# Kernel optimization log

Measured on AMD Instinct MI355X. Metric: run time of the kernel, lower is better.

## Reference

```python
import jax, jax.numpy as jnp
import numpy as np
import math

B, DSET, DOUT, DH, H, L, M, C = 32, 512, 16, 1024, 16, 6, 127, 8
S = M + 1            # sos + maximum_components targets
DHEAD = DH // H
DIN = DSET + 1 + 2 * DOUT  # embedding input dim = 545
DTOK = 1 + 2 * DOUT        # per-step token dim = 33


def _pos_encoding(max_len, d):
    pos = np.arange(max_len, dtype=np.float32)[:, None]
    div = np.exp(np.arange(0, d, 2, dtype=np.float32) * (-math.log(10000.0) / d))
    pe = np.zeros((max_len, d), dtype=np.float32)
    pe[:, 0::2] = np.sin(pos * div)
    pe[:, 1::2] = np.cos(pos * div)
    return jnp.asarray(pe[None])  # [1, max_len, d]


def setup_inputs() -> dict:
    key = jax.random.key(0)
    ks = iter(jax.random.split(key, 64))
    def n(shape, s=0.02):
        return jax.random.normal(next(ks), shape, jnp.float32) * s
    return {
        "input": jax.random.normal(next(ks), (B, DSET), jnp.float32),
        "targets": jax.random.normal(next(ks), (B, M, DTOK), jnp.float32),
        "W_emb": n((DH, DIN)), "b_emb": jnp.zeros((DH,), jnp.float32),
        "sos": jax.random.normal(next(ks), (1, 1, DTOK), jnp.float32),
        "Wqkv": n((L, 3 * DH, DH)), "bqkv": jnp.zeros((L, 3 * DH), jnp.float32),
        "Wo": n((L, DH, DH)), "bo": jnp.zeros((L, DH), jnp.float32),
        "W1": n((L, DH, DH)), "b1": jnp.zeros((L, DH), jnp.float32),
        "W2": n((L, DH, DH)), "b2": jnp.zeros((L, DH), jnp.float32),
        "g1": jnp.ones((L, DH), jnp.float32), "be1": jnp.zeros((L, DH), jnp.float32),
        "g2": jnp.ones((L, DH), jnp.float32), "be2": jnp.zeros((L, DH), jnp.float32),
        "Wm": n((1, DH)), "bm": jnp.zeros((1,), jnp.float32),
        "Wpi_m": n((C, DH)), "bpi_m": jnp.zeros((C,), jnp.float32),
        "Wmu_m": n((C * DOUT, DH)), "bmu_m": jnp.zeros((C * DOUT,), jnp.float32),
        "Wsg_m": n((C * DOUT, DH)), "bsg_m": jnp.zeros((C * DOUT,), jnp.float32),
        "Wpi_v": n((C, DH)), "bpi_v": jnp.zeros((C,), jnp.float32),
        "Wmu_v": n((C * DOUT, DH)), "bmu_v": jnp.zeros((C * DOUT,), jnp.float32),
        "Wsg_v": n((C * DOUT, DH)), "bsg_v": jnp.zeros((C * DOUT,), jnp.float32),
    }


def _ln(x, g, b, eps=1e-5):
    m = x.mean(-1, keepdims=True)
    v = ((x - m) ** 2).mean(-1, keepdims=True)
    return (x - m) / jnp.sqrt(v + eps) * g + b


def _layer(x, Wqkv, bqkv, Wo, bo, W1, b1, W2, b2, g1, be1, g2, be2, causal):
    # PyTorch TransformerEncoderLayer (post-norm, relu, dropout=0)
    qkv = x @ Wqkv.T + bqkv                       # [B,S,3*DH]
    q, k, v = jnp.split(qkv, 3, axis=-1)
    q = q.reshape(B, -1, H, DHEAD)
    k = k.reshape(B, -1, H, DHEAD)
    v = v.reshape(B, -1, H, DHEAD)
    sc = jnp.einsum('bqhd,bkhd->bhqk', q, k) / math.sqrt(DHEAD)
    sc = jnp.where(causal, sc, -1e30)
    a = jax.nn.softmax(sc, -1)
    o = jnp.einsum('bhqk,bkhd->bqhd', a, v).reshape(B, -1, DH)
    x = _ln(x + o @ Wo.T + bo, g1, be1)
    ff = jax.nn.relu(x @ W1.T + b1) @ W2.T + b2
    return _ln(x + ff, g2, be2)


def _mdn(h, Wpi, bpi, Wmu, bmu, Wsg, bsg):
    pi = jax.nn.softmax(h @ Wpi.T + bpi, -1)                      # [B,M,C]
    mu = (h @ Wmu.T + bmu).reshape(h.shape[:-1] + (C, DOUT))      # [B,M,C,DOUT]
    var = jnp.exp(h @ Wsg.T + bsg).reshape(h.shape[:-1] + (C, DOUT))
    return pi, mu, var


def reference(input, targets, W_emb, b_emb, sos, Wqkv, bqkv, Wo, bo, W1, b1, W2, b2,
              g1, be1, g2, be2, Wm, bm, Wpi_m, bpi_m, Wmu_m, bmu_m, Wsg_m, bsg_m,
              Wpi_v, bpi_v, Wmu_v, bmu_v, Wsg_v, bsg_v):
    pe = _pos_encoding(3 * M, DH)
    tokens = jnp.broadcast_to(sos, (B, 1, DTOK))
    cond = jnp.broadcast_to(input[:, None, :], (B, S, DSET))
    seq = jnp.concatenate([tokens, targets], axis=1)              # [B,S,DTOK]
    x = jnp.concatenate([cond, seq], axis=-1) @ W_emb.T + b_emb
    x = x + pe[:, :S, :]
    causal = jnp.tril(jnp.ones((S, S), bool))[None, None]
    for i in range(L):
        x = _layer(x, Wqkv[i], bqkv[i], Wo[i], bo[i], W1[i], b1[i], W2[i], b2[i],
                   g1[i], be1[i], g2[i], be2[i], causal)
    h = x[:, :-1, :]                                              # [B,M,DH]
    masks = h @ Wm.T + bm                                         # [B,M,1]
    pi_m, mu_m, var_m = _mdn(h, Wpi_m, bpi_m, Wmu_m, bmu_m, Wsg_m, bsg_m)
    pi_v, mu_v, var_v = _mdn(h, Wpi_v, bpi_v, Wmu_v, bmu_v, Wsg_v, bsg_v)
    return (pi_m, mu_m, var_m, pi_v, mu_v, var_v, masks)
```

## Files before the change

kernel.cpp:

```cpp
#include <hip/hip_runtime.h>
#include <hip/hip_bf16.h>

typedef __hip_bfloat16 bf16;
typedef __attribute__((ext_vector_type(8))) short bfrag8;
typedef __attribute__((ext_vector_type(4))) float facc4;
typedef __attribute__((ext_vector_type(4))) unsigned short us4;
typedef __attribute__((ext_vector_type(8))) unsigned short us8;
typedef __attribute__((ext_vector_type(4))) float f32x4;

#define AS1C const __attribute__((address_space(1))) void
#define AS3  __attribute__((address_space(3))) void

__device__ __forceinline__ void gload_lds16(const void* src, void* dst) {
    __builtin_amdgcn_global_load_lds((AS1C*)src, (AS3*)dst, 16, 0, 0);
}

__device__ __forceinline__ unsigned short f2bf(float f) {
    unsigned u = __float_as_uint(f);
    unsigned r = u + 0x7FFFu + ((u >> 16) & 1u);
    return (unsigned short)(r >> 16);
}
__device__ __forceinline__ float bf2f(unsigned short u) {
    return __uint_as_float((unsigned)u << 16);
}

__global__ void prep_cvt_kernel(const float* __restrict__ input, const float* __restrict__ targets,
                                const float* __restrict__ sos, const float* __restrict__ W_emb,
                                const float* __restrict__ Wm, const float* __restrict__ Wpi_m,
                                const float* __restrict__ Wmu_m, const float* __restrict__ Wsg_m,
                                const float* __restrict__ Wpi_v, const float* __restrict__ Wmu_v,
                                const float* __restrict__ Wsg_v,
                                const float* __restrict__ bm, const float* __restrict__ bpi_m,
                                const float* __restrict__ bmu_m, const float* __restrict__ bsg_m,
                                const float* __restrict__ bpi_v, const float* __restrict__ bmu_v,
                                const float* __restrict__ bsg_v,
                                const float* __restrict__ Wqkv, const float* __restrict__ Wo,
                                const float* __restrict__ W1, const float* __restrict__ W2,
                                float* __restrict__ pe, bf16* __restrict__ xin,
                                bf16* __restrict__ wemb, bf16* __restrict__ whead,
                                float* __restrict__ bhead,
                                bf16* __restrict__ wqb, bf16* __restrict__ wob,
                                bf16* __restrict__ w1b, bf16* __restrict__ w2b) {
    int bid = blockIdx.x;
    int t = threadIdx.x;
    if (bid < 4608) {
        int l = bid / 768;
        int s = bid - l * 768;
        const float* src; bf16* dst;
        if (s < 384)      { src = Wqkv + (size_t)l * 3145728; dst = wqb + (size_t)l * 3145728; }
        else if (s < 512) { src = Wo + (size_t)l * 1048576; dst = wob + (size_t)l * 1048576; s -= 384; }
        else if (s < 640) { src = W1 + (size_t)l * 1048576; dst = w1b + (size_t)l * 1048576; s -= 512; }
        else              { src = W2 + (size_t)l * 1048576; dst = w2b + (size_t)l * 1048576; s -= 640; }
        size_t pbase = (size_t)s * 1024 + t;
#pragma unroll
        for (int it = 0; it < 4; ++it) {
            size_t o = (pbase + it * 256) * 8;
            const f32x4* p = (const f32x4*)(src + o);
            f32x4 v1 = __builtin_nontemporal_load(p);
            f32x4 v2 = __builtin_nontemporal_load(p + 1);
            us8 w8;
            w8[0] = f2bf(v1.x); w8[1] = f2bf(v1.y); w8[2] = f2bf(v1.z); w8[3] = f2bf(v1.w);
            w8[4] = f2bf(v2.x); w8[5] = f2bf(v2.y); w8[6] = f2bf(v2.z); w8[7] = f2bf(v2.w);
            *(us8*)(dst + o) = w8;
        }
    } else if (bid < 4736) {
        int s = bid - 4608;
        float4 v;
#pragma unroll
        for (int j = 0; j < 4; ++j) {
            int c = t * 4 + j;
            int i = c >> 1;
            float div = expf(-9.210340371976184f * (float)(2 * i) * (1.f / 1024.f));
            float a = (float)s * div;
            v[j] = (c & 1) ? cosf(a) : sinf(a);
        }
        *(float4*)(pe + (size_t)s * 1024 + t * 4) = v;
    } else if (bid < 5888) {
        int chunk = (bid - 4736) * 256 + t;
        int row = chunk / 72;
        int cc = chunk - row * 72;
        int b = row >> 7, s = row & 127;
        us8 w8;
        if (cc < 64) {
            const float* p = input + (size_t)b * 512 + cc * 8;
            float4 v1 = *(const float4*)p;
            float4 v2 = *(const float4*)(p + 4);
            w8[0] = f2bf(v1.x); w8[1] = f2bf(v1.y); w8[2] = f2bf(v1.z); w8[3] = f2bf(v1.w);
            w8[4] = f2bf(v2.x); w8[5] = f2bf(v2.y); w8[6] = f2bf(v2.z); w8[7] = f2bf(v2.w);
        } else {
#pragma unroll
            for (int j = 0; j < 8; ++j) {
                int col = cc * 8 + j;
                float v = 0.f;
                if (col < 545) {
                    int jj = col - 512;
                    v = (s == 0) ? sos[jj] : targets[((size_t)b * 127 + (s - 1)) * 33 + jj];
                }
                w8[j] = f2bf(v);
            }
        }
        *(us8*)(xin + (size_t)row * 576 + cc * 8) = w8;
    } else if (bid < 6176) {
        int chunk = (bid - 5888) * 256 + t;
        int row = chunk / 72;
        int cc = chunk - row * 72;
        us8 w8;
#pragma unroll
        for (int j = 0; j < 8; ++j) {
            int col = cc * 8 + j;
            w8[j] = f2bf(col < 545 ? W_emb[(size_t)row * 545 + col] : 0.f);
        }
        *(us8*)(wemb + (size_t)row * 576 + cc * 8) = w8;
    } else if (bid < 6496) {
        int chunk = (bid - 6176) * 256 + t;
        int r = chunk >> 7;
        int cc = chunk & 127;
        const float* wsrc = nullptr; int off = 0;
        if (r == 0)        { wsrc = Wm;    off = 0; }
        else if (r < 9)    { wsrc = Wpi_m; off = r - 1; }
        else if (r < 137)  { wsrc = Wmu_m; off = r - 9; }
        else if (r < 265)  { wsrc = Wsg_m; off = r - 137; }
        else if (r < 273)  { wsrc = Wpi_v; off = r - 265; }
        else if (r < 401)  { wsrc = Wmu_v; off = r - 273; }
        else if (r < 529)  { wsrc = Wsg_v; off = r - 401; }
        us8 w8;
        if (wsrc) {
            const float* p = wsrc + (size_t)off * 1024 + cc * 8;
            float4 v1 = *(const float4*)p;
            float4 v2 = *(const float4*)(p + 4);
            w8[0] = f2bf(v1.x); w8[1] = f2bf(v1.y); w8[2] = f2bf(v1.z); w8[3] = f2bf(v1.w);
            w8[4] = f2bf(v2.x); w8[5] = f2bf(v2.y); w8[6] = f2bf(v2.z); w8[7] = f2bf(v2.w);
        } else {
#pragma unroll
            for (int j = 0; j < 8; ++j) w8[j] = 0;
        }
        *(us8*)(whead + (size_t)r * 1024 + cc * 8) = w8;
    } else {
        if (t < 529) {
            const float* bsrc; int off;
            if (t == 0)       { bsrc = bm;    off = 0; }
            else if (t < 9)   { bsrc = bpi_m; off = t - 1; }
            else if (t < 137) { bsrc = bmu_m; off = t - 9; }
            else if (t < 265) { bsrc = bsg_m; off = t - 137; }
            else if (t < 273) { bsrc = bpi_v; off = t - 265; }
            else if (t < 401) { bsrc = bmu_v; off = t - 273; }
            else              { bsrc = bsg_v; off = t - 401; }
            bhead[t] = bsrc[off];
        }
    }
}

template<int EPI, int CFG>
__global__ __launch_bounds__(CFG ? 512 : 256, CFG ? 2 : 3) void gemm_bt(
    const bf16* __restrict__ A, const bf16* __restrict__ Bw,
    float* __restrict__ Cf, bf16* __restrict__ Cb,
    const float* __restrict__ bias, const float* __restrict__ pe,
    int M, int N, int K, int lda, int ldb, int ldc, long long Az, long long Cz)
{
    constexpr int NT  = CFG ? 512 : 256;
    constexpr int NB  = CFG ? 2 : 1;
    constexpr int MI  = CFG ? 2 : 4;
    constexpr int BK  = (CFG == 2) ? 128 : 64;
    constexpr int RB  = BK * 2;
    constexpr int CPR = BK / 8;
    constexpr int NCH = (128 * CPR) / NT;
    constexpr int KS  = BK / 32;
    __shared__ __align__(16) bf16 sA[NB][128 * BK];
    __shared__ __align__(16) bf16 sB[NB][128 * BK];
    const int t = threadIdx.x;
    const int w = t >> 6, la = t & 63;
    const int wm = CFG ? (w >> 1) * 32 : (w >> 1) * 64;
    const int wn = (w & 1) * 64;
    const int m0 = blockIdx.y * 128, n0 = blockIdx.x * 128;
    const int z = blockIdx.z;
    A += (long long)z * Az;

    facc4 zero4 = {0.f, 0.f, 0.f, 0.f};
    facc4 acc[MI][4];
#pragma unroll
    for (int mi = 0; mi < MI; ++mi)
#pragma unroll
        for (int ni = 0; ni < 4; ++ni) acc[mi][ni] = zero4;

    auto stage = [&](int buf, int kt) {
#pragma unroll
        for (int i = 0; i < NCH; ++i) {
            int c = i * NT + t;
            int r = c / CPR;
            int cc = c - r * CPR;
            int bc = (cc * 16) ^ ((r & 7) << 4);
            gload_lds16(A + (size_t)(m0 + r) * lda + kt + (bc >> 1),
                        (char*)sA[buf] + (size_t)c * 16);
            gload_lds16(Bw + (size_t)(n0 + r) * ldb + kt + (bc >> 1),
                        (char*)sB[buf] + (size_t)c * 16);
        }
    };
    auto compute = [&](int buf) {
#pragma unroll
        for (int ks = 0; ks < KS; ++ks) {
            bfrag8 af[MI], bfv[4];
            const int koffb = (ks * 32 + (la >> 4) * 8) * 2;
#pragma unroll
            for (int i = 0; i < MI; ++i) {
                int rowa = wm + i * 16 + (la & 15);
                af[i] = *(const bfrag8*)((const char*)sA[buf] + rowa * RB + (koffb ^ ((rowa & 7) << 4)));
            }
#pragma unroll
            for (int i = 0; i < 4; ++i) {
                int rowb = wn + i * 16 + (la & 15);
                bfv[i] = *(const bfrag8*)((const char*)sB[buf] + rowb * RB + (koffb ^ ((rowb & 7) << 4)));
            }
#pragma unroll
            for (int mi = 0; mi < MI; ++mi)
#pragma unroll
                for (int ni = 0; ni < 4; ++ni)
                    acc[mi][ni] = __builtin_amdgcn_mfma_f32_16x16x32_bf16(bfv[ni], af[mi], acc[mi][ni], 0, 0, 0);
        }
    };

    const int nk = K / BK;
    if constexpr (CFG) {
        stage(0, 0);
        __syncthreads();
        int cur = 0;
        for (int kt = 0; kt < nk; ++kt) {
            if (kt + 1 < nk) stage(cur ^ 1, (kt + 1) * BK);
            compute(cur);
            __syncthreads();
            cur ^= 1;
        }
    } else {
        for (int kt = 0; kt < nk; ++kt) {
            stage(0, kt * BK);
            __syncthreads();
            compute(0);
            __syncthreads();
        }
    }
#pragma unroll
    for (int mi = 0; mi < MI; ++mi) {
        int row = m0 + wm + mi * 16 + (la & 15);
#pragma unroll
        for (int ni = 0; ni < 4; ++ni) {
            int colb = n0 + wn + ni * 16 + (la >> 4) * 4;
            if constexpr (EPI == 3) {
                if (row >= M) continue;
#pragma unroll
                for (int j = 0; j < 4; ++j) {
                    int col = colb + j;
                    if (col < N)
                        Cf[(size_t)z * Cz + (size_t)row * ldc + col] = acc[mi][ni][j] + bias[col];
                }
            } else {
                float4 bv = *(const float4*)(bias + colb);
                facc4 v = acc[mi][ni];
                v[0] += bv.x; v[1] += bv.y; v[2] += bv.z; v[3] += bv.w;
                size_t cidx = (size_t)row * ldc + colb;
                if constexpr (EPI == 0) {
                    us4 o; o.x = f2bf(v[0]); o.y = f2bf(v[1]); o.z = f2bf(v[2]); o.w = f2bf(v[3]);
                    *(us4*)(Cb + cidx) = o;
                } else if constexpr (EPI == 1) {
                    us4 o;
                    o.x = f2bf(v[0] > 0.f ? v[0] : 0.f); o.y = f2bf(v[1] > 0.f ? v[1] : 0.f);
                    o.z = f2bf(v[2] > 0.f ? v[2] : 0.f); o.w = f2bf(v[3] > 0.f ? v[3] : 0.f);
                    *(us4*)(Cb + cidx) = o;
                } else {
                    float4 p = *(const float4*)(pe + (size_t)(row & 127) * 1024 + colb);
                    us4 o;
                    o.x = f2bf(v[0] + p.x); o.y = f2bf(v[1] + p.y);
                    o.z = f2bf(v[2] + p.z); o.w = f2bf(v[3] + p.w);
                    *(us4*)(Cb + cidx) = o;
                }
            }
        }
    }
}

__global__ __launch_bounds__(256) void attn_fused(const bf16* __restrict__ qkv, bf16* __restrict__ obf)
{
    __shared__ __align__(16) char lds[65536];
    char* sQ  = lds;
    char* sK  = lds + 16384;
    char* sS  = lds + 32768;
    char* sVT = lds;
    float* redm = (float*)(lds + 16384);
    float* reds = (float*)(lds + 16384 + 1024);

    const int t = threadIdx.x, w = t >> 6, la = t & 63;
    const int b = blockIdx.x >> 4, h = blockIdx.x & 15;
    const size_t base = (size_t)b * 128 * 3072 + (size_t)h * 64;

#pragma unroll
    for (int i = 0; i < 4; ++i) {
        int c = i * 256 + w * 64 + la;
        int r = c >> 3;
        int bc = ((c & 7) * 16) ^ ((r & 7) << 4);
        gload_lds16(qkv + base + (size_t)r * 3072 + (bc >> 1),
                    sQ + (size_t)(i * 256 + w * 64) * 16);
        gload_lds16(qkv + base + 1024 + (size_t)r * 3072 + (bc >> 1),
                    sK + (size_t)(i * 256 + w * 64) * 16);
    }
    __syncthreads();

    const int wm = (w >> 1) * 64, wn = (w & 1) * 64;
    facc4 zero4 = {0.f, 0.f, 0.f, 0.f};
    facc4 acc[4][4];
#pragma unroll
    for (int mi = 0; mi < 4; ++mi)
#pragma unroll
        for (int ni = 0; ni < 4; ++ni) acc[mi][ni] = zero4;
#pragma unroll
    for (int ks = 0; ks < 2; ++ks) {
        bfrag8 af[4], bfv[4];
        const int koffb = (ks * 32 + (la >> 4) * 8) * 2;
#pragma unroll
        for (int i = 0; i < 4; ++i) {
            int rowa = wm + i * 16 + (la & 15);
            af[i] = *(const bfrag8*)(sQ + rowa * 128 + (koffb ^ ((rowa & 7) << 4)));
            int rowb = wn + i * 16 + (la & 15);
            bfv[i] = *(const bfrag8*)(sK + rowb * 128 + (koffb ^ ((rowb & 7) << 4)));
        }
#pragma unroll
        for (int mi = 0; mi < 4; ++mi)
#pragma unroll
            for (int ni = 0; ni < 4; ++ni)
                acc[mi][ni] = __builtin_amdgcn_mfma_f32_16x16x32_bf16(bfv[ni], af[mi], acc[mi][ni], 0, 0, 0);
    }
    __syncthreads();

#pragma unroll
    for (int i = 0; i < 4; ++i) {
        int c = i * 256 + t;
        int r = c >> 3;
        int d0 = (c & 7) * 8;
        bfrag8 vv = *(const bfrag8*)(qkv + base + 2048 + (size_t)r * 3072 + d0);
#pragma unroll
        for (int j = 0; j < 8; ++j) {
            int d = d0 + j;
            *(short*)(sVT + d * 256 + ((2 * r) ^ ((d & 7) << 4))) = vv[j];
        }
    }

    const int colh = (w & 1) * 128;
    float tmp4[4];
#pragma unroll
    for (int mi = 0; mi < 4; ++mi) {
        int q = wm + mi * 16 + (la & 15);
        float mx = -1e30f;
#pragma unroll
        for (int ni = 0; ni < 4; ++ni) {
            int kb = wn + ni * 16 + (la >> 4) * 4;
#pragma unroll
            for (int j = 0; j < 4; ++j) {
                float s = acc[mi][ni][j] * 0.125f;
                acc[mi][ni][j] = s;
                if (kb + j <= q) mx = fmaxf(mx, s);
            }
        }
        mx = fmaxf(mx, __shfl_xor(mx, 16));
        mx = fmaxf(mx, __shfl_xor(mx, 32));
        tmp4[mi] = mx;
    }
    if ((la >> 4) == 0) {
#pragma unroll
        for (int mi = 0; mi < 4; ++mi) redm[colh + wm + mi * 16 + la] = tmp4[mi];
    }
    __syncthreads();
#pragma unroll
    for (int mi = 0; mi < 4; ++mi) {
        int q = wm + mi * 16 + (la & 15);
        float m = fmaxf(redm[q], redm[128 + q]);
        float sm = 0.f;
#pragma unroll
        for (int ni = 0; ni < 4; ++ni) {
            int kb = wn + ni * 16 + (la >> 4) * 4;
#pragma unroll
            for (int j = 0; j < 4; ++j) {
                float e = (kb + j <= q) ? __expf(acc[mi][ni][j] - m) : 0.f;
                acc[mi][ni][j] = e;
                sm += e;
            }
        }
        sm += __shfl_xor(sm, 16);
        sm += __shfl_xor(sm, 32);
        tmp4[mi] = sm;
    }
    __syncthreads();
    if ((la >> 4) == 0) {
#pragma unroll
        for (int mi = 0; mi < 4; ++mi) reds[colh + wm + mi * 16 + la] = tmp4[mi];
    }
    __syncthreads();
#pragma unroll
    for (int mi = 0; mi < 4; ++mi) {
        int q = wm + mi * 16 + (la & 15);
        float inv = 1.f / (reds[q] + reds[128 + q]);
#pragma unroll
        for (int ni = 0; ni < 4; ++ni) {
            int kb = wn + ni * 16 + (la >> 4) * 4;
            us4 sv;
            sv.x = f2bf(acc[mi][ni][0] * inv); sv.y = f2bf(acc[mi][ni][1] * inv);
            sv.z = f2bf(acc[mi][ni][2] * inv); sv.w = f2bf(acc[mi][ni][3] * inv);
            *(us4*)(sS + q * 256 + ((2 * kb) ^ ((q & 7) << 4))) = sv;
        }
    }
    __syncthreads();

    const int wm2 = (w >> 1) * 64, wn2 = (w & 1) * 32;
    facc4 a2[4][2];
#pragma unroll
    for (int mi = 0; mi < 4; ++mi) { a2[mi][0] = zero4; a2[mi][1] = zero4; }
#pragma unroll
    for (int ks = 0; ks < 4; ++ks) {
        bfrag8 pa[4], vb[2];
        const int koffb = (ks * 32 + (la >> 4) * 8) * 2;
#pragma unroll
        for (int mi = 0; mi < 4; ++mi) {
            int rowa = wm2 + mi * 16 + (la & 15);
            pa[mi] = *(const bfrag8*)(sS + rowa * 256 + (koffb ^ ((rowa & 7) << 4)));
        }
#pragma unroll
        for (int ni = 0; ni < 2; ++ni) {
            int rowb = wn2 + ni * 16 + (la & 15);
            vb[ni] = *(const bfrag8*)(sVT + rowb * 256 + (koffb ^ ((rowb & 7) << 4)));
        }
#pragma unroll
        for (int mi = 0; mi < 4; ++mi)
#pragma unroll
            for (int ni = 0; ni < 2; ++ni)
                a2[mi][ni] = __builtin_amdgcn_mfma_f32_16x16x32_bf16(vb[ni], pa[mi], a2[mi][ni], 0, 0, 0);
    }
#pragma unroll
    for (int mi = 0; mi < 4; ++mi) {
        int s = wm2 + mi * 16 + (la & 15);
#pragma unroll
        for (int ni = 0; ni < 2; ++ni) {
            int db = wn2 + ni * 16 + (la >> 4) * 4;
            us4 ov;
            ov.x = f2bf(a2[mi][ni][0]); ov.y = f2bf(a2[mi][ni][1]);
            ov.z = f2bf(a2[mi][ni][2]); ov.w = f2bf(a2[mi][ni][3]);
            *(us4*)(obf + ((size_t)(b * 128 + s)) * 1024 + h * 64 + db) = ov;
        }
    }
}

__global__ __launch_bounds__(256) void ln_res_kernel(const bf16* __restrict__ go,
                                                     const bf16* __restrict__ res,
                                                     const float* __restrict__ g, const float* __restrict__ be,
                                                     bf16* __restrict__ xb_out)
{
    const int row = blockIdx.x, t = threadIdx.x;
    size_t o = (size_t)row * 1024 + t * 4;
    us4 gv4 = *(const us4*)(go + o);
    us4 rv4 = *(const us4*)(res + o);
    float t0 = bf2f(rv4.x) + bf2f(gv4.x);
    float t1 = bf2f(rv4.y) + bf2f(gv4.y);
    float t2 = bf2f(rv4.z) + bf2f(gv4.z);
    float t3 = bf2f(rv4.w) + bf2f(gv4.w);
    float s = t0 + t1 + t2 + t3;
    float q = t0 * t0 + t1 * t1 + t2 * t2 + t3 * t3;
#pragma unroll
    for (int off = 32; off; off >>= 1) {
        s += __shfl_xor(s, off);
        q += __shfl_xor(q, off);
    }
    __shared__ float ssum[4], sqs[4];
    if ((t & 63) == 0) { ssum[t >> 6] = s; sqs[t >> 6] = q; }
    __syncthreads();
    s = ssum[0] + ssum[1] + ssum[2] + ssum[3];
    q = sqs[0] + sqs[1] + sqs[2] + sqs[3];
    float mean = s * (1.f / 1024.f);
    float var = q * (1.f / 1024.f) - mean * mean;
    float rstd = rsqrtf(var + 1e-5f);
    float4 gv = *(const float4*)(g + t * 4);
    float4 bv = *(const float4*)(be + t * 4);
    float o0 = (t0 - mean) * rstd * gv.x + bv.x;
    float o1 = (t1 - mean) * rstd * gv.y + bv.y;
    float o2 = (t2 - mean) * rstd * gv.z + bv.z;
    float o3 = (t3 - mean) * rstd * gv.w + bv.w;
    us4 obv; obv.x = f2bf(o0); obv.y = f2bf(o1); obv.z = f2bf(o2); obv.w = f2bf(o3);
    *(us4*)(xb_out + o) = obv;
}

__global__ void finalize_kernel(const float* __restrict__ hout, float* __restrict__ out) {
    const size_t O_PI_M = 0, O_MU_M = 32512, O_VAR_M = 552704, O_PI_V = 1072896,
                 O_MU_V = 1105408, O_VAR_V = 1625600, O_MASK = 2145792;
    int rm = blockIdx.x;
    const float* hrow = hout + (size_t)rm * 529;
    int t = threadIdx.x;
    if (t < 128) {
        out[O_MU_M  + (size_t)rm * 128 + t] = hrow[9 + t];
        out[O_VAR_M + (size_t)rm * 128 + t] = expf(hrow[137 + t]);
        out[O_MU_V  + (size_t)rm * 128 + t] = hrow[273 + t];
        out[O_VAR_V + (size_t)rm * 128 + t] = expf(hrow[401 + t]);
    } else if (t == 128) {
        out[O_MASK + rm] = hrow[0];
    } else if (t == 129 || t == 130) {
        int boff = (t == 129) ? 1 : 265;
        size_t oo = ((t == 129) ? O_PI_M : O_PI_V) + (size_t)rm * 8;
        float v[8], mx = -1e30f;
#pragma unroll
        for (int j = 0; j < 8; ++j) { v[j] = hrow[boff + j]; mx = fmaxf(mx, v[j]); }
        float sm = 0.f;
#pragma unroll
        for (int j = 0; j < 8; ++j) { v[j] = expf(v[j] - mx); sm += v[j]; }
        float inv = 1.f / sm;
#pragma unroll
        for (int j = 0; j < 8; ++j) out[oo + j] = v[j] * inv;
    }
}

extern "C" void kernel_launch(void* const* d_in, const int* in_sizes, int n_in,
                              void* d_out, int out_size, void* d_ws, size_t ws_size,
                              hipStream_t stream) {
    (void)in_sizes; (void)n_in; (void)out_size; (void)ws_size;
    const float* input   = (const float*)d_in[0];
    const float* targets = (const float*)d_in[1];
    const float* W_emb   = (const float*)d_in[2];
    const float* b_emb   = (const float*)d_in[3];
    const float* sos     = (const float*)d_in[4];
    const float* Wqkv    = (const float*)d_in[5];
    const float* bqkv    = (const float*)d_in[6];
    const float* Wo      = (const float*)d_in[7];
    const float* bo      = (const float*)d_in[8];
    const float* W1      = (const float*)d_in[9];
    const float* b1      = (const float*)d_in[10];
    const float* W2      = (const float*)d_in[11];
    const float* b2      = (const float*)d_in[12];
    const float* g1      = (const float*)d_in[13];
    const float* be1     = (const float*)d_in[14];
    const float* g2      = (const float*)d_in[15];
    const float* be2     = (const float*)d_in[16];
    const float* Wm      = (const float*)d_in[17];
    const float* bm      = (const float*)d_in[18];
    const float* Wpi_m   = (const float*)d_in[19];
    const float* bpi_m   = (const float*)d_in[20];
    const float* Wmu_m   = (const float*)d_in[21];
    const float* bmu_m   = (const float*)d_in[22];
    const float* Wsg_m   = (const float*)d_in[23];
    const float* bsg_m   = (const float*)d_in[24];
    const float* Wpi_v   = (const float*)d_in[25];
    const float* bpi_v   = (const float*)d_in[26];
    const float* Wmu_v   = (const float*)d_in[27];
    const float* bmu_v   = (const float*)d_in[28];
    const float* Wsg_v   = (const float*)d_in[29];
    const float* bsg_v   = (const float*)d_in[30];
    float* out = (float*)d_out;

    char* ws = (char*)d_ws;
    float* pe      = (float*)(ws + 0);
    bf16*  xin     = (bf16*)(ws + 524288);
    bf16*  wemb    = (bf16*)(ws + 5242880);
    bf16*  whead   = (bf16*)(ws + 6422528);
    float* bhead   = (float*)(ws + 7733248);
    bf16*  xb      = (bf16*)(ws + 24513024);
    bf16*  qkvb    = (bf16*)(ws + 32901632);
    bf16*  ob      = (bf16*)(ws + 58067456);
    bf16*  tmpb    = (bf16*)(ws + 66456064);
    bf16*  wqb_all = (bf16*)(ws + 83233280);
    bf16*  wob_all = (bf16*)(ws + 120982016);
    bf16*  w1b_all = (bf16*)(ws + 133564928);
    bf16*  w2b_all = (bf16*)(ws + 146147840);
    float* hout    = (float*)(ws + 158730752);

    prep_cvt_kernel<<<6497, 256, 0, stream>>>(input, targets, sos, W_emb,
                                              Wm, Wpi_m, Wmu_m, Wsg_m, Wpi_v, Wmu_v, Wsg_v,
                                              bm, bpi_m, bmu_m, bsg_m, bpi_v, bmu_v, bsg_v,
                                              Wqkv, Wo, W1, W2,
                                              pe, xin, wemb, whead, bhead,
                                              wqb_all, wob_all, w1b_all, w2b_all);
    gemm_bt<4, 1><<<dim3(8, 32, 1), 512, 0, stream>>>(xin, wemb, nullptr, xb, b_emb, pe,
                                                      4096, 1024, 576, 576, 576, 1024, 0, 0);
    for (int l = 0; l < 6; ++l) {
        const bf16* wqb = wqb_all + (size_t)l * 3145728;
        const bf16* wob = wob_all + (size_t)l * 1048576;
        const bf16* w1b = w1b_all + (size_t)l * 1048576;
        const bf16* w2b = w2b_all + (size_t)l * 1048576;
        gemm_bt<0, 0><<<dim3(24, 32, 1), 256, 0, stream>>>(xb, wqb, nullptr, qkvb, bqkv + l * 3072,
                                                           nullptr, 4096, 3072, 1024, 1024, 1024, 3072, 0, 0);
        attn_fused<<<512, 256, 0, stream>>>(qkvb, ob);
        gemm_bt<0, 2><<<dim3(8, 32, 1), 512, 0, stream>>>(ob, wob, nullptr, tmpb, bo + l * 1024,
                                                          nullptr, 4096, 1024, 1024, 1024, 1024, 1024, 0, 0);
        ln_res_kernel<<<4096, 256, 0, stream>>>(tmpb, xb, g1 + l * 1024, be1 + l * 1024, xb);
        gemm_bt<1, 2><<<dim3(8, 32, 1), 512, 0, stream>>>(xb, w1b, nullptr, ob, b1 + l * 1024,
                                                          nullptr, 4096, 1024, 1024, 1024, 1024, 1024, 0, 0);
        gemm_bt<0, 2><<<dim3(8, 32, 1), 512, 0, stream>>>(ob, w2b, nullptr, tmpb, b2 + l * 1024,
                                                          nullptr, 4096, 1024, 1024, 1024, 1024, 1024, 0, 0);
        ln_res_kernel<<<4096, 256, 0, stream>>>(tmpb, xb, g2 + l * 1024, be2 + l * 1024, xb);
    }
    gemm_bt<3, 2><<<dim3(5, 1, 32), 512, 0, stream>>>(xb, whead, hout, nullptr, bhead, nullptr,
                                                      127, 529, 1024, 1024, 1024, 529, 131072LL, 67183LL);
    finalize_kernel<<<4064, 256, 0, stream>>>(hout, out);
}
```

Measured before the change: 741.2 us.

## Merge softmax reductions, widen layernorm rows per block, raise QKV GEMM occupancy

The attention softmax now computes per-half row max and sum in one pass and merges the two halves with an online-softmax rescale. This removes one LDS round trip and two block barriers. The residual-layernorm kernel processes two rows per 256-thread block with 8-element vector loads, halving the grid. The QKV GEMM launch bound moves from 3 to 4 waves per SIMD, which may force register spills.

```diff
diff --git a/kernel.cpp b/kernel.cpp
--- a/kernel.cpp
+++ b/kernel.cpp
@@ -151,7 +151,7 @@
 }
 
 template<int EPI, int CFG>
-__global__ __launch_bounds__(CFG ? 512 : 256, CFG ? 2 : 3) void gemm_bt(
+__global__ __launch_bounds__(CFG ? 512 : 256, CFG ? 2 : 4) void gemm_bt(
     const bf16* __restrict__ A, const bf16* __restrict__ Bw,
     float* __restrict__ Cf, bf16* __restrict__ Cb,
     const float* __restrict__ bias, const float* __restrict__ pe,
@@ -342,7 +342,7 @@
     }
 
     const int colh = (w & 1) * 128;
-    float tmp4[4];
+    float tmpm[4], tmps[4];
 #pragma unroll
     for (int mi = 0; mi < 4; ++mi) {
         int q = wm + mi * 16 + (la & 15);
@@ -359,48 +359,42 @@
         }
         mx = fmaxf(mx, __shfl_xor(mx, 16));
         mx = fmaxf(mx, __shfl_xor(mx, 32));
-        tmp4[mi] = mx;
-    }
-    if ((la >> 4) == 0) {
-#pragma unroll
-        for (int mi = 0; mi < 4; ++mi) redm[colh + wm + mi * 16 + la] = tmp4[mi];
-    }
-    __syncthreads();
-#pragma unroll
-    for (int mi = 0; mi < 4; ++mi) {
-        int q = wm + mi * 16 + (la & 15);
-        float m = fmaxf(redm[q], redm[128 + q]);
         float sm = 0.f;
 #pragma unroll
         for (int ni = 0; ni < 4; ++ni) {
             int kb = wn + ni * 16 + (la >> 4) * 4;
 #pragma unroll
             for (int j = 0; j < 4; ++j) {
-                float e = (kb + j <= q) ? __expf(acc[mi][ni][j] - m) : 0.f;
+                float e = (kb + j <= q) ? __expf(acc[mi][ni][j] - mx) : 0.f;
                 acc[mi][ni][j] = e;
                 sm += e;
             }
         }
         sm += __shfl_xor(sm, 16);
         sm += __shfl_xor(sm, 32);
-        tmp4[mi] = sm;
-    }
-    __syncthreads();
+        tmpm[mi] = mx; tmps[mi] = sm;
+    }
     if ((la >> 4) == 0) {
 #pragma unroll
-        for (int mi = 0; mi < 4; ++mi) reds[colh + wm + mi * 16 + la] = tmp4[mi];
+        for (int mi = 0; mi < 4; ++mi) {
+            redm[colh + wm + mi * 16 + la] = tmpm[mi];
+            reds[colh + wm + mi * 16 + la] = tmps[mi];
+        }
     }
     __syncthreads();
 #pragma unroll
     for (int mi = 0; mi < 4; ++mi) {
         int q = wm + mi * 16 + (la & 15);
-        float inv = 1.f / (reds[q] + reds[128 + q]);
+        float m0 = redm[q], m1 = redm[128 + q];
+        float M = fmaxf(m0, m1);
+        float tot = reds[q] * __expf(m0 - M) + reds[128 + q] * __expf(m1 - M);
+        float sc = __expf(tmpm[mi] - M) / tot;
 #pragma unroll
         for (int ni = 0; ni < 4; ++ni) {
             int kb = wn + ni * 16 + (la >> 4) * 4;
             us4 sv;
-            sv.x = f2bf(acc[mi][ni][0] * inv); sv.y = f2bf(acc[mi][ni][1] * inv);
-            sv.z = f2bf(acc[mi][ni][2] * inv); sv.w = f2bf(acc[mi][ni][3] * inv);
+            sv.x = f2bf(acc[mi][ni][0] * sc); sv.y = f2bf(acc[mi][ni][1] * sc);
+            sv.z = f2bf(acc[mi][ni][2] * sc); sv.w = f2bf(acc[mi][ni][3] * sc);
             *(us4*)(sS + q * 256 + ((2 * kb) ^ ((q & 7) << 4))) = sv;
         }
     }
@@ -449,16 +443,20 @@
                                                      const float* __restrict__ g, const float* __restrict__ be,
                                                      bf16* __restrict__ xb_out)
 {
-    const int row = blockIdx.x, t = threadIdx.x;
-    size_t o = (size_t)row * 1024 + t * 4;
-    us4 gv4 = *(const us4*)(go + o);
-    us4 rv4 = *(const us4*)(res + o);
-    float t0 = bf2f(rv4.x) + bf2f(gv4.x);
-    float t1 = bf2f(rv4.y) + bf2f(gv4.y);
-    float t2 = bf2f(rv4.z) + bf2f(gv4.z);
-    float t3 = bf2f(rv4.w) + bf2f(gv4.w);
-    float s = t0 + t1 + t2 + t3;
-    float q = t0 * t0 + t1 * t1 + t2 * t2 + t3 * t3;
+    const int t = threadIdx.x;
+    const int row = blockIdx.x * 2 + (t >> 7);
+    const int ct = t & 127;
+    size_t o = (size_t)row * 1024 + ct * 8;
+    us8 gv8 = *(const us8*)(go + o);
+    us8 rv8 = *(const us8*)(res + o);
+    float v[8];
+    float s = 0.f, q = 0.f;
+#pragma unroll
+    for (int j = 0; j < 8; ++j) {
+        v[j] = bf2f(rv8[j]) + bf2f(gv8[j]);
+        s += v[j];
+        q += v[j] * v[j];
+    }
 #pragma unroll
     for (int off = 32; off; off >>= 1) {
         s += __shfl_xor(s, off);
@@ -467,19 +465,23 @@
     __shared__ float ssum[4], sqs[4];
     if ((t & 63) == 0) { ssum[t >> 6] = s; sqs[t >> 6] = q; }
     __syncthreads();
-    s = ssum[0] + ssum[1] + ssum[2] + ssum[3];
-    q = sqs[0] + sqs[1] + sqs[2] + sqs[3];
+    int rb = (t >> 7) * 2;
+    s = ssum[rb] + ssum[rb + 1];
+    q = sqs[rb] + sqs[rb + 1];
     float mean = s * (1.f / 1024.f);
     float var = q * (1.f / 1024.f) - mean * mean;
     float rstd = rsqrtf(var + 1e-5f);
-    float4 gv = *(const float4*)(g + t * 4);
-    float4 bv = *(const float4*)(be + t * 4);
-    float o0 = (t0 - mean) * rstd * gv.x + bv.x;
-    float o1 = (t1 - mean) * rstd * gv.y + bv.y;
-    float o2 = (t2 - mean) * rstd * gv.z + bv.z;
-    float o3 = (t3 - mean) * rstd * gv.w + bv.w;
-    us4 obv; obv.x = f2bf(o0); obv.y = f2bf(o1); obv.z = f2bf(o2); obv.w = f2bf(o3);
-    *(us4*)(xb_out + o) = obv;
+    float4 g1v = *(const float4*)(g + ct * 8);
+    float4 g2v = *(const float4*)(g + ct * 8 + 4);
+    float4 b1v = *(const float4*)(be + ct * 8);
+    float4 b2v = *(const float4*)(be + ct * 8 + 4);
+    float ga[8] = {g1v.x, g1v.y, g1v.z, g1v.w, g2v.x, g2v.y, g2v.z, g2v.w};
+    float ba[8] = {b1v.x, b1v.y, b1v.z, b1v.w, b2v.x, b2v.y, b2v.z, b2v.w};
+    us8 ob;
+#pragma unroll
+    for (int j = 0; j < 8; ++j)
+        ob[j] = f2bf((v[j] - mean) * rstd * ga[j] + ba[j]);
+    *(us8*)(xb_out + o) = ob;
 }
 
 __global__ void finalize_kernel(const float* __restrict__ hout, float* __restrict__ out) {
@@ -581,12 +583,12 @@
         attn_fused<<<512, 256, 0, stream>>>(qkvb, ob);
         gemm_bt<0, 2><<<dim3(8, 32, 1), 512, 0, stream>>>(ob, wob, nullptr, tmpb, bo + l * 1024,
                                                           nullptr, 4096, 1024, 1024, 1024, 1024, 1024, 0, 0);
-        ln_res_kernel<<<4096, 256, 0, stream>>>(tmpb, xb, g1 + l * 1024, be1 + l * 1024, xb);
+        ln_res_kernel<<<2048, 256, 0, stream>>>(tmpb, xb, g1 + l * 1024, be1 + l * 1024, xb);
         gemm_bt<1, 2><<<dim3(8, 32, 1), 512, 0, stream>>>(xb, w1b, nullptr, ob, b1 + l * 1024,
                                                           nullptr, 4096, 1024, 1024, 1024, 1024, 1024, 0, 0);
         gemm_bt<0, 2><<<dim3(8, 32, 1), 512, 0, stream>>>(ob, w2b, nullptr, tmpb, b2 + l * 1024,
                                                           nullptr, 4096, 1024, 1024, 1024, 1024, 1024, 0, 0);
-        ln_res_kernel<<<4096, 256, 0, stream>>>(tmpb, xb, g2 + l * 1024, be2 + l * 1024, xb);
+        ln_res_kernel<<<2048, 256, 0, stream>>>(tmpb, xb, g2 + l * 1024, be2 + l * 1024, xb);
     }
     gemm_bt<3, 2><<<dim3(5, 1, 32), 512, 0, stream>>>(xb, whead, hout, nullptr, bhead, nullptr,
                                                       127, 529, 1024, 1024, 1024, 529, 131072LL, 67183LL);
```

Measured after the change: 732.4 us. No clear change (-1.2%).
